# Optimization experiments

Measured on AMD Instinct MI355X. Metric: run time of the kernel, lower is better.

## Reference

```python
import jax, jax.numpy as jnp
import numpy as np

NB_CAT = 8192       # nb_category per column
RANK = 16           # low-rank factor dimension
N_COLS = 4          # number of categorical columns (len(embedding_sizes))
N_PAIRS = 1048576   # number of (x, y) index pairs
FRAC_DIAG = 0.9     # fraction_diagonal init


def setup_inputs() -> dict:
    key = jax.random.key(0)
    k1, k2, k3, k4 = jax.random.split(key, 4)
    x = jax.random.randint(k1, (N_PAIRS, N_COLS), 0, NB_CAT, dtype=jnp.int32)
    y = jax.random.randint(k2, (N_PAIRS, N_COLS), 0, NB_CAT, dtype=jnp.int32)
    # params initialized as in the torch module, plus small noise so values are non-degenerate
    std = (FRAC_DIAG * jnp.ones((N_COLS, NB_CAT), dtype=jnp.float32)
           + 0.01 * jax.random.normal(k3, (N_COLS, NB_CAT), dtype=jnp.float32))
    covar_factor = ((1.0 - FRAC_DIAG) / np.float32(np.sqrt(RANK))
                    * jnp.ones((N_COLS, NB_CAT, RANK), dtype=jnp.float32)
                    + 0.01 * jax.random.normal(k4, (N_COLS, NB_CAT, RANK), dtype=jnp.float32))
    return {"x": x, "y": y, "covar_factor": covar_factor, "std": std}


def reference(x, y, covar_factor, std):
    # Build full covariance per column: F @ F.T + diag(std^2)   -> [C, N, N]
    cov = jnp.einsum('cnr,cmr->cnm', covar_factor, covar_factor)
    diag_idx = jnp.arange(cov.shape[1])
    cov = cov.at[:, diag_idx, diag_idx].add(std * std)
    # Gather requested (x, y) entries per column, then reduce (should_reduce=True)
    cols = jnp.arange(cov.shape[0])  # [C]
    vals = cov[cols[None, :], x, y]  # [B, C]
    return vals.sum(axis=-1)         # [B]
```

## Files before the change

### kernel.cpp

```cpp
#include <hip/hip_runtime.h>

#define NB_CAT  8192
#define RANK    16
#define N_COLS  4
#define N_PAIRS 1048576

#define SLICE_BYTES (NB_CAT * 16)
#define TBL_BYTES   ((size_t)N_COLS * SLICE_BYTES)
#define LDS_BYTES   (128 * 1024)

typedef float float2v __attribute__((ext_vector_type(2)));

#if defined(__HIP_DEVICE_COMPILE__) && defined(__has_builtin)
#if __has_builtin(__builtin_amdgcn_cvt_pk_f32_fp8) && __has_builtin(__builtin_amdgcn_cvt_pk_fp8_f32)
#define DEV_FP8_HW 1
#endif
#if __has_builtin(__builtin_amdgcn_global_load_lds)
#define DEV_GLL 1
#endif
#endif

template <int C> __device__ __forceinline__ int comp(const int4& v) {
    if (C == 0) return v.x;
    if (C == 1) return v.y;
    if (C == 2) return v.z;
    return v.w;
}

__device__ __forceinline__ float sw_dec_fp8(unsigned int b) {
    const unsigned int s = b >> 7, e = (b >> 3) & 0xF, m = b & 7;
    float v;
    if (e == 0) v = (float)m * 0.001953125f;
    else        v = ldexpf((float)(8 + m), (int)e - 10);
    return s ? -v : v;
}
__device__ __forceinline__ unsigned int sw_enc_fp8(float f) {
    const unsigned int s = (__float_as_uint(f) >> 31) << 7;
    float a = fabsf(f);
    if (a > 448.f) a = 448.f;
    float q;
    if (a >= 0.015625f) {
        int ex; const float m = frexpf(a, &ex);
        q = ldexpf(rintf(ldexpf(m, 4)), ex - 4);
    } else {
        q = rintf(a * 512.f) * 0.001953125f;
    }
    if (q == 0.f) return s;
    int ex; const float m = frexpf(q, &ex);
    if (ex - 1 < -6) {
        const unsigned int mm = (unsigned int)rintf(q * 512.f);
        return s | (mm & 7);
    }
    const unsigned int e = (unsigned int)(ex - 1 + 7);
    const unsigned int mm = (unsigned int)rintf(ldexpf(m, 4)) & 7;
    return s | (e << 3) | mm;
}

template <bool HI>
__device__ __forceinline__ float2v dec2(unsigned int u) {
#ifdef DEV_FP8_HW
    return __builtin_amdgcn_cvt_pk_f32_fp8((int)u, HI);
#else
    const unsigned int w = HI ? (u >> 16) : u;
    float2v r;
    r.x = sw_dec_fp8(w & 0xFF);
    r.y = sw_dec_fp8((w >> 8) & 0xFF);
    return r;
#endif
}

__device__ __forceinline__ float dot8_fp8(uint2 A, uint2 B, float acc) {
#define TERM(u, v, SEL)                                                        \
    {                                                                          \
        const float2v a = dec2<SEL>((u));                                      \
        const float2v b = dec2<SEL>((v));                                      \
        acc = fmaf(a.x, b.x, acc);                                             \
        acc = fmaf(a.y, b.y, acc);                                             \
    }
    TERM(A.x, B.x, false) TERM(A.x, B.x, true)
    TERM(A.y, B.y, false) TERM(A.y, B.y, true)
#undef TERM
    return acc;
}

__global__ __launch_bounds__(256) void pack_fp8_kernel(
    const float4* __restrict__ src, uint4* __restrict__ dst)
{
    const int r = blockIdx.x * 256 + threadIdx.x;
    const float4 f0 = src[r * 4 + 0];
    const float4 f1 = src[r * 4 + 1];
    const float4 f2 = src[r * 4 + 2];
    const float4 f3 = src[r * 4 + 3];
    uint4 u;
#ifdef DEV_FP8_HW
    int w;
    w = 0;
    w = __builtin_amdgcn_cvt_pk_fp8_f32(f0.x, f0.y, w, false);
    w = __builtin_amdgcn_cvt_pk_fp8_f32(f0.z, f0.w, w, true);
    u.x = (unsigned int)w;
    w = 0;
    w = __builtin_amdgcn_cvt_pk_fp8_f32(f1.x, f1.y, w, false);
    w = __builtin_amdgcn_cvt_pk_fp8_f32(f1.z, f1.w, w, true);
    u.y = (unsigned int)w;
    w = 0;
    w = __builtin_amdgcn_cvt_pk_fp8_f32(f2.x, f2.y, w, false);
    w = __builtin_amdgcn_cvt_pk_fp8_f32(f2.z, f2.w, w, true);
    u.z = (unsigned int)w;
    w = 0;
    w = __builtin_amdgcn_cvt_pk_fp8_f32(f3.x, f3.y, w, false);
    w = __builtin_amdgcn_cvt_pk_fp8_f32(f3.z, f3.w, w, true);
    u.w = (unsigned int)w;
#else
    u.x = sw_enc_fp8(f0.x) | (sw_enc_fp8(f0.y) << 8) | (sw_enc_fp8(f0.z) << 16) | (sw_enc_fp8(f0.w) << 24);
    u.y = sw_enc_fp8(f1.x) | (sw_enc_fp8(f1.y) << 8) | (sw_enc_fp8(f1.z) << 16) | (sw_enc_fp8(f1.w) << 24);
    u.z = sw_enc_fp8(f2.x) | (sw_enc_fp8(f2.y) << 8) | (sw_enc_fp8(f2.z) << 16) | (sw_enc_fp8(f2.w) << 24);
    u.w = sw_enc_fp8(f3.x) | (sw_enc_fp8(f3.y) << 8) | (sw_enc_fp8(f3.z) << 16) | (sw_enc_fp8(f3.w) << 24);
#endif
    const int c = r >> 13;
    const int a = r & (NB_CAT - 1);
    uint2* d2 = (uint2*)dst;
    uint2 w01; w01.x = u.x; w01.y = u.y;
    uint2 w23; w23.x = u.z; w23.y = u.w;
    d2[(c << 14) + a]        = w01;
    d2[(c << 14) + 8192 + a] = w23;
}

__global__ __launch_bounds__(1024, 1) void IndexKernel_32238024524411_kernel(
    const int4*  __restrict__ x4,
    const int4*  __restrict__ y4,
    const uint4* __restrict__ tbl,
    const float* __restrict__ stdv,
    float*       __restrict__ out)
{
    extern __shared__ uint4 sh4[];

    const int tid  = threadIdx.x;
    const int base = blockIdx.x * 4096 + tid;

#ifdef DEV_GLL
#define STAGE(K)                                                               \
    {                                                                          \
        const uint4* s_ = tbl + (size_t)(K) * 4096;                            \
        uint4* d_ = sh4 + (((K) & 1) ? 4096 : 0);                              \
        _Pragma("unroll")                                                      \
        for (int it = 0; it < 4; ++it) {                                       \
            __builtin_amdgcn_global_load_lds(                                  \
                (const __attribute__((address_space(1))) unsigned int*)(s_ + it * 1024 + tid), \
                (__attribute__((address_space(3))) unsigned int*)(d_ + it * 1024 + tid),       \
                16, 0, 0);                                                     \
        }                                                                      \
    }
#else
#define STAGE(K)                                                               \
    {                                                                          \
        const uint4* s_ = tbl + (size_t)(K) * 4096;                            \
        uint4* d_ = sh4 + (((K) & 1) ? 4096 : 0);                              \
        _Pragma("unroll")                                                      \
        for (int it = 0; it < 4; ++it) d_[it * 1024 + tid] = s_[it * 1024 + tid]; \
    }
#endif

    STAGE(0) STAGE(1)

    int4 xv[4], yv[4];
#pragma unroll
    for (int j = 0; j < 4; ++j) {
        xv[j] = x4[base + j * 1024];
        yv[j] = y4[base + j * 1024];
    }

    float acc[4] = {0.f, 0.f, 0.f, 0.f};

#pragma unroll
    for (int j = 0; j < 4; ++j) {
        const int4 a = xv[j], b = yv[j];
        if (a.x == b.x) { const float s = stdv[0 * NB_CAT + a.x]; acc[j] = fmaf(s, s, acc[j]); }
        if (a.y == b.y) { const float s = stdv[1 * NB_CAT + a.y]; acc[j] = fmaf(s, s, acc[j]); }
        if (a.z == b.z) { const float s = stdv[2 * NB_CAT + a.z]; acc[j] = fmaf(s, s, acc[j]); }
        if (a.w == b.w) { const float s = stdv[3 * NB_CAT + a.w]; acc[j] = fmaf(s, s, acc[j]); }
    }

    asm volatile("s_waitcnt vmcnt(0) lgkmcnt(0)" ::: "memory");
    __builtin_amdgcn_s_barrier();
    asm volatile("" ::: "memory");

#define GATHER(K)                                                              \
    {                                                                          \
        constexpr int c_ = (K) >> 1;                                           \
        const uint2* bp = (const uint2*)(sh4 + (((K) & 1) ? 4096 : 0));        \
        _Pragma("unroll")                                                      \
        for (int j = 0; j < 4; ++j) {                                          \
            const int a_ = comp<c_>(xv[j]);                                    \
            const int b_ = comp<c_>(yv[j]);                                    \
            const uint2 Av = bp[a_];                                           \
            const uint2 Bv = bp[b_];                                           \
            acc[j] = dot8_fp8(Av, Bv, acc[j]);                                 \
        }                                                                      \
    }

#define SYNC_REFILL(KNEXT)                                                     \
    __builtin_amdgcn_s_barrier();                                              \
    asm volatile("" ::: "memory");                                             \
    STAGE(KNEXT)                                                               \
    asm volatile("s_waitcnt vmcnt(4)" ::: "memory");                           \
    __builtin_amdgcn_s_barrier();                                              \
    asm volatile("" ::: "memory");

    GATHER(0)
    SYNC_REFILL(2)
    GATHER(1)
    SYNC_REFILL(3)
    GATHER(2)
    SYNC_REFILL(4)
    GATHER(3)
    SYNC_REFILL(5)
    GATHER(4)
    SYNC_REFILL(6)
    GATHER(5)
    SYNC_REFILL(7)
    GATHER(6)
    __builtin_amdgcn_s_barrier();
    asm volatile("s_waitcnt vmcnt(0)" ::: "memory");
    __builtin_amdgcn_s_barrier();
    asm volatile("" ::: "memory");
    GATHER(7)

#undef SYNC_REFILL
#undef GATHER
#undef STAGE

#pragma unroll
    for (int j = 0; j < 4; ++j) {
        out[base + j * 1024] = acc[j];
    }
}

__global__ __launch_bounds__(256) void fallback_kernel(
    const int* __restrict__ x, const int* __restrict__ y,
    const float4* __restrict__ cf, const float* __restrict__ stdv,
    float* __restrict__ out)
{
    const int tid = threadIdx.x;
    const int q = tid & 15, gi = tid >> 4, c = q >> 2, s = q & 3;
    const int p0 = blockIdx.x * 32 + gi, p1 = p0 + 16;
    const int rb = c * NB_CAT;
    const int xi0 = x[p0*4+c], yi0 = y[p0*4+c], xi1 = x[p1*4+c], yi1 = y[p1*4+c];
    const float4 a0 = cf[(size_t)(rb+xi0)*4 + s], b0 = cf[(size_t)(rb+yi0)*4 + s];
    const float4 a1 = cf[(size_t)(rb+xi1)*4 + s], b1 = cf[(size_t)(rb+yi1)*4 + s];
    float v0 = a0.x*b0.x; v0 = fmaf(a0.y,b0.y,v0); v0 = fmaf(a0.z,b0.z,v0); v0 = fmaf(a0.w,b0.w,v0);
    float v1 = a1.x*b1.x; v1 = fmaf(a1.y,b1.y,v1); v1 = fmaf(a1.z,b1.z,v1); v1 = fmaf(a1.w,b1.w,v1);
    if (s == 0 && xi0 == yi0) { float sd = stdv[rb+xi0]; v0 = fmaf(sd,sd,v0); }
    if (s == 0 && xi1 == yi1) { float sd = stdv[rb+yi1]; v1 = fmaf(sd,sd,v1); }
    int t;
    t = __builtin_amdgcn_update_dpp(0, __float_as_int(v0), 0xB1, 0xF, 0xF, true); v0 += __int_as_float(t);
    t = __builtin_amdgcn_update_dpp(0, __float_as_int(v0), 0x4E, 0xF, 0xF, true); v0 += __int_as_float(t);
    t = __builtin_amdgcn_update_dpp(0, __float_as_int(v0), 0x141,0xF, 0xF, true); v0 += __int_as_float(t);
    t = __builtin_amdgcn_update_dpp(0, __float_as_int(v0), 0x128,0xF, 0xF, true); v0 += __int_as_float(t);
    t = __builtin_amdgcn_update_dpp(0, __float_as_int(v1), 0xB1, 0xF, 0xF, true); v1 += __int_as_float(t);
    t = __builtin_amdgcn_update_dpp(0, __float_as_int(v1), 0x4E, 0xF, 0xF, true); v1 += __int_as_float(t);
    t = __builtin_amdgcn_update_dpp(0, __float_as_int(v1), 0x141,0xF, 0xF, true); v1 += __int_as_float(t);
    t = __builtin_amdgcn_update_dpp(0, __float_as_int(v1), 0x128,0xF, 0xF, true); v1 += __int_as_float(t);
    if (q == 0) { out[p0] = v0; out[p1] = v1; }
}

extern "C" void kernel_launch(void* const* d_in, const int* in_sizes, int n_in,
                              void* d_out, int out_size, void* d_ws, size_t ws_size,
                              hipStream_t stream) {
    const int*   x    = (const int*)d_in[0];
    const int*   y    = (const int*)d_in[1];
    const float* cf   = (const float*)d_in[2];
    const float* stdv = (const float*)d_in[3];
    float*       out  = (float*)d_out;

    if (ws_size < TBL_BYTES) {
        fallback_kernel<<<N_PAIRS / 32, 256, 0, stream>>>(
            x, y, (const float4*)cf, stdv, out);
        return;
    }

    (void)hipFuncSetAttribute(
        reinterpret_cast<const void*>(&IndexKernel_32238024524411_kernel),
        hipFuncAttributeMaxDynamicSharedMemorySize, LDS_BYTES);

    pack_fp8_kernel<<<N_COLS * NB_CAT / 256, 256, 0, stream>>>(
        (const float4*)cf, (uint4*)d_ws);

    IndexKernel_32238024524411_kernel<<<N_PAIRS / 4096, 1024, LDS_BYTES, stream>>>(
        (const int4*)x, (const int4*)y, (const uint4*)d_ws, stdv, out);
}
```

Baseline: 88.56 us.

## Split FP8 table into quarter-rank slices for smaller LDS and two blocks per CU

```diff
diff --git a/kernel.cpp b/kernel.cpp
--- a/kernel.cpp
+++ b/kernel.cpp
@@ -5,9 +5,9 @@
 #define N_COLS  4
 #define N_PAIRS 1048576
 
-#define SLICE_BYTES (NB_CAT * 16)
-#define TBL_BYTES   ((size_t)N_COLS * SLICE_BYTES)
-#define LDS_BYTES   (128 * 1024)
+#define TBL_BYTES   ((size_t)N_COLS * NB_CAT * 16)
+#define QSLICE_U4   2048
+#define LDS_BYTES   (64 * 1024)
 
 typedef float float2v __attribute__((ext_vector_type(2)));
 
@@ -69,7 +69,7 @@
 #endif
 }
 
-__device__ __forceinline__ float dot8_fp8(uint2 A, uint2 B, float acc) {
+__device__ __forceinline__ float dot4_fp8(unsigned int A, unsigned int B, float acc) {
 #define TERM(u, v, SEL)                                                        \
     {                                                                          \
         const float2v a = dec2<SEL>((u));                                      \
@@ -77,14 +77,13 @@
         acc = fmaf(a.x, b.x, acc);                                             \
         acc = fmaf(a.y, b.y, acc);                                             \
     }
-    TERM(A.x, B.x, false) TERM(A.x, B.x, true)
-    TERM(A.y, B.y, false) TERM(A.y, B.y, true)
+    TERM(A, B, false) TERM(A, B, true)
 #undef TERM
     return acc;
 }
 
 __global__ __launch_bounds__(256) void pack_fp8_kernel(
-    const float4* __restrict__ src, uint4* __restrict__ dst)
+    const float4* __restrict__ src, unsigned int* __restrict__ dstw)
 {
     const int r = blockIdx.x * 256 + threadIdx.x;
     const float4 f0 = src[r * 4 + 0];
@@ -118,14 +117,14 @@
 #endif
     const int c = r >> 13;
     const int a = r & (NB_CAT - 1);
-    uint2* d2 = (uint2*)dst;
-    uint2 w01; w01.x = u.x; w01.y = u.y;
-    uint2 w23; w23.x = u.z; w23.y = u.w;
-    d2[(c << 14) + a]        = w01;
-    d2[(c << 14) + 8192 + a] = w23;
-}
-
-__global__ __launch_bounds__(1024, 1) void IndexKernel_32238024524411_kernel(
+    const int base = (c << 15) + a;
+    dstw[base]             = u.x;
+    dstw[base + 1 * 8192]  = u.y;
+    dstw[base + 2 * 8192]  = u.z;
+    dstw[base + 3 * 8192]  = u.w;
+}
+
+__global__ __launch_bounds__(512, 4) void IndexKernel_32238024524411_kernel(
     const int4*  __restrict__ x4,
     const int4*  __restrict__ y4,
     const uint4* __restrict__ tbl,
@@ -135,28 +134,28 @@
     extern __shared__ uint4 sh4[];
 
     const int tid  = threadIdx.x;
-    const int base = blockIdx.x * 4096 + tid;
+    const int base = blockIdx.x * 2048 + tid;
 
 #ifdef DEV_GLL
 #define STAGE(K)                                                               \
     {                                                                          \
-        const uint4* s_ = tbl + (size_t)(K) * 4096;                            \
-        uint4* d_ = sh4 + (((K) & 1) ? 4096 : 0);                              \
+        const uint4* s_ = tbl + (size_t)(K) * QSLICE_U4;                       \
+        uint4* d_ = sh4 + (((K) & 1) ? QSLICE_U4 : 0);                         \
         _Pragma("unroll")                                                      \
         for (int it = 0; it < 4; ++it) {                                       \
             __builtin_amdgcn_global_load_lds(                                  \
-                (const __attribute__((address_space(1))) unsigned int*)(s_ + it * 1024 + tid), \
-                (__attribute__((address_space(3))) unsigned int*)(d_ + it * 1024 + tid),       \
+                (const __attribute__((address_space(1))) unsigned int*)(s_ + it * 512 + tid), \
+                (__attribute__((address_space(3))) unsigned int*)(d_ + it * 512 + tid),       \
                 16, 0, 0);                                                     \
         }                                                                      \
     }
 #else
 #define STAGE(K)                                                               \
     {                                                                          \
-        const uint4* s_ = tbl + (size_t)(K) * 4096;                            \
-        uint4* d_ = sh4 + (((K) & 1) ? 4096 : 0);                              \
+        const uint4* s_ = tbl + (size_t)(K) * QSLICE_U4;                       \
+        uint4* d_ = sh4 + (((K) & 1) ? QSLICE_U4 : 0);                         \
         _Pragma("unroll")                                                      \
-        for (int it = 0; it < 4; ++it) d_[it * 1024 + tid] = s_[it * 1024 + tid]; \
+        for (int it = 0; it < 4; ++it) d_[it * 512 + tid] = s_[it * 512 + tid]; \
     }
 #endif
 
@@ -165,8 +164,8 @@
     int4 xv[4], yv[4];
 #pragma unroll
     for (int j = 0; j < 4; ++j) {
-        xv[j] = x4[base + j * 1024];
-        yv[j] = y4[base + j * 1024];
+        xv[j] = x4[base + j * 512];
+        yv[j] = y4[base + j * 512];
     }
 
     float acc[4] = {0.f, 0.f, 0.f, 0.f};
@@ -186,15 +185,16 @@
 
 #define GATHER(K)                                                              \
     {                                                                          \
-        constexpr int c_ = (K) >> 1;                                           \
-        const uint2* bp = (const uint2*)(sh4 + (((K) & 1) ? 4096 : 0));        \
+        constexpr int c_ = (K) >> 2;                                           \
+        const unsigned int* bp =                                               \
+            (const unsigned int*)(sh4 + (((K) & 1) ? QSLICE_U4 : 0));          \
         _Pragma("unroll")                                                      \
         for (int j = 0; j < 4; ++j) {                                          \
             const int a_ = comp<c_>(xv[j]);                                    \
             const int b_ = comp<c_>(yv[j]);                                    \
-            const uint2 Av = bp[a_];                                           \
-            const uint2 Bv = bp[b_];                                           \
-            acc[j] = dot8_fp8(Av, Bv, acc[j]);                                 \
+            const unsigned int Av = bp[a_];                                    \
+            const unsigned int Bv = bp[b_];                                    \
+            acc[j] = dot4_fp8(Av, Bv, acc[j]);                                 \
         }                                                                      \
     }
 
@@ -206,24 +206,26 @@
     __builtin_amdgcn_s_barrier();                                              \
     asm volatile("" ::: "memory");
 
-    GATHER(0)
-    SYNC_REFILL(2)
-    GATHER(1)
-    SYNC_REFILL(3)
-    GATHER(2)
-    SYNC_REFILL(4)
-    GATHER(3)
-    SYNC_REFILL(5)
-    GATHER(4)
-    SYNC_REFILL(6)
-    GATHER(5)
-    SYNC_REFILL(7)
-    GATHER(6)
+    GATHER(0)  SYNC_REFILL(2)
+    GATHER(1)  SYNC_REFILL(3)
+    GATHER(2)  SYNC_REFILL(4)
+    GATHER(3)  SYNC_REFILL(5)
+    GATHER(4)  SYNC_REFILL(6)
+    GATHER(5)  SYNC_REFILL(7)
+    GATHER(6)  SYNC_REFILL(8)
+    GATHER(7)  SYNC_REFILL(9)
+    GATHER(8)  SYNC_REFILL(10)
+    GATHER(9)  SYNC_REFILL(11)
+    GATHER(10) SYNC_REFILL(12)
+    GATHER(11) SYNC_REFILL(13)
+    GATHER(12) SYNC_REFILL(14)
+    GATHER(13) SYNC_REFILL(15)
+    GATHER(14)
     __builtin_amdgcn_s_barrier();
     asm volatile("s_waitcnt vmcnt(0)" ::: "memory");
     __builtin_amdgcn_s_barrier();
     asm volatile("" ::: "memory");
-    GATHER(7)
+    GATHER(15)
 
 #undef SYNC_REFILL
 #undef GATHER
@@ -231,7 +233,7 @@
 
 #pragma unroll
     for (int j = 0; j < 4; ++j) {
-        out[base + j * 1024] = acc[j];
+        out[base + j * 512] = acc[j];
     }
 }
 
@@ -283,8 +285,8 @@
         hipFuncAttributeMaxDynamicSharedMemorySize, LDS_BYTES);
 
     pack_fp8_kernel<<<N_COLS * NB_CAT / 256, 256, 0, stream>>>(
-        (const float4*)cf, (uint4*)d_ws);
-
-    IndexKernel_32238024524411_kernel<<<N_PAIRS / 4096, 1024, LDS_BYTES, stream>>>(
+        (const float4*)cf, (unsigned int*)d_ws);
+
+    IndexKernel_32238024524411_kernel<<<N_PAIRS / 2048, 512, LDS_BYTES, stream>>>(
         (const int4*)x, (const int4*)y, (const uint4*)d_ws, stdv, out);
 }
```

Result: slower. 91.61 us (+3.4%).
